# Optimization experiments

Measured on AMD Instinct MI355X. Metric: run time of the kernel, lower is better.

The kernel has to match this reference:

```python
import jax, jax.numpy as jnp
import numpy as np

NUM_HEADS = 16
NUM_KV_HEADS = 8
HEAD_DIM = 128
EPS = 1e-6
SLIDING_WINDOW = 1024
ROPE_THETA = 10000.0


def _rms_norm(x, w):
    # per-head RMSNorm in fp32, as in Qwen3RMSNorm
    xf = x.astype(jnp.float32)
    var = jnp.mean(xf * xf, axis=-1, keepdims=True)
    return (w * (xf * jax.lax.rsqrt(var + EPS))).astype(x.dtype)


def _rotate_half(x):
    d = x.shape[-1] // 2
    return jnp.concatenate([-x[..., d:], x[..., :d]], axis=-1)


def setup_inputs() -> dict:
    key = jax.random.key(0)
    ks = jax.random.split(key, 6)
    B, S, H = 2, 2048, 2048
    hidden_states = jax.random.normal(ks[0], (B, S, H), dtype=jnp.float32)
    # RoPE tables per HF convention: cos/sin of shape [B, S, head_dim]
    inv_freq = 1.0 / (ROPE_THETA ** (np.arange(0, HEAD_DIM, 2, dtype=np.float32) / HEAD_DIM))
    pos = np.arange(S, dtype=np.float32)
    ang = np.outer(pos, inv_freq)  # [S, HEAD_DIM/2]
    emb = np.concatenate([ang, ang], axis=-1)  # [S, HEAD_DIM]
    cos = jnp.broadcast_to(jnp.asarray(np.cos(emb)), (B, S, HEAD_DIM))
    sin = jnp.broadcast_to(jnp.asarray(np.sin(emb)), (B, S, HEAD_DIM))
    sc = 0.02
    Wq = jax.random.normal(ks[1], (NUM_HEADS * HEAD_DIM, H), dtype=jnp.float32) * sc
    Wk = jax.random.normal(ks[2], (NUM_KV_HEADS * HEAD_DIM, H), dtype=jnp.float32) * sc
    Wv = jax.random.normal(ks[3], (NUM_KV_HEADS * HEAD_DIM, H), dtype=jnp.float32) * sc
    Wo = jax.random.normal(ks[4], (H, NUM_HEADS * HEAD_DIM), dtype=jnp.float32) * sc
    q_norm_w = jnp.ones((HEAD_DIM,), dtype=jnp.float32)
    k_norm_w = jnp.ones((HEAD_DIM,), dtype=jnp.float32)
    return {"hidden_states": hidden_states, "cos": cos, "sin": sin,
            "Wq": Wq, "Wk": Wk, "Wv": Wv, "Wo": Wo,
            "q_norm_w": q_norm_w, "k_norm_w": k_norm_w}


def reference(hidden_states, cos, sin, Wq, Wk, Wv, Wo, q_norm_w, k_norm_w):
    B, S, H = hidden_states.shape
    scaling = HEAD_DIM ** -0.5
    # projections (torch Linear: y = x @ W.T), reshape to [B, nH, S, D]
    q = jnp.einsum('bsh,oh->bso', hidden_states, Wq).reshape(B, S, NUM_HEADS, HEAD_DIM)
    k = jnp.einsum('bsh,oh->bso', hidden_states, Wk).reshape(B, S, NUM_KV_HEADS, HEAD_DIM)
    v = jnp.einsum('bsh,oh->bso', hidden_states, Wv).reshape(B, S, NUM_KV_HEADS, HEAD_DIM)
    q = _rms_norm(q, q_norm_w).transpose(0, 2, 1, 3)  # [B, nH, S, D]
    k = _rms_norm(k, k_norm_w).transpose(0, 2, 1, 3)  # [B, nKV, S, D]
    v = v.transpose(0, 2, 1, 3)
    # RoPE, cos/sin broadcast over heads (unsqueeze_dim=1)
    c = cos[:, None, :, :]
    s = sin[:, None, :, :]
    q = q * c + _rotate_half(q) * s
    k = k * c + _rotate_half(k) * s
    # GQA: repeat kv heads
    groups = NUM_HEADS // NUM_KV_HEADS
    k = jnp.repeat(k, groups, axis=1)
    v = jnp.repeat(v, groups, axis=1)
    # causal + sliding-window mask
    i = jnp.arange(S)[:, None]
    j = jnp.arange(S)[None, :]
    mask = (j <= i) & (i - j < SLIDING_WINDOW)  # [S, S]
    scores = jnp.einsum('bhqd,bhkd->bhqk', q, k) * scaling
    scores = jnp.where(mask[None, None], scores, jnp.finfo(scores.dtype).min)
    probs = jax.nn.softmax(scores, axis=-1)
    attn = jnp.einsum('bhqk,bhkd->bhqd', probs, v)  # [B, nH, S, D]
    attn = attn.transpose(0, 2, 1, 3).reshape(B, S, NUM_HEADS * HEAD_DIM)
    out = jnp.einsum('bso,ho->bsh', attn, Wo)
    return out
```

## Files before the change

### kernel.cpp

```cpp
#include <hip/hip_runtime.h>
#include <stdint.h>

#define S_LEN 2048
#define BATCH 2
#define HID 2048
#define NH 16
#define NKV 8
#define HD 128
#define WINDOW 1024
#define SCALE 0.08838834764831845f
#define QKVW 4096

typedef unsigned short u16;
typedef unsigned int u32;
typedef __attribute__((ext_vector_type(8))) short short8;
typedef __attribute__((ext_vector_type(4))) float f32x4;
typedef __attribute__((ext_vector_type(16))) float f32x16;
typedef __attribute__((ext_vector_type(4))) u16 u16x4;

__device__ __forceinline__ u16 f2b(float f) {
  u32 u = __builtin_bit_cast(u32, f);
  return (u16)((u + 0x7fffu + ((u >> 16) & 1u)) >> 16);
}
__device__ __forceinline__ float b2f(u16 h) {
  u32 u = ((u32)h) << 16;
  return __builtin_bit_cast(float, u);
}
__device__ __forceinline__ u32 pk_bf16(float a, float b) {
  u32 d;
  asm("v_cvt_pk_bf16_f32 %0, %1, %2" : "=v"(d) : "v"(a), "v"(b));
  return d;
}

__device__ __forceinline__ void gload_lds16(const u16* g, u16* l) {
  __builtin_amdgcn_global_load_lds(
      (const __attribute__((address_space(1))) u32*)g,
      (__attribute__((address_space(3))) u32*)l, 16, 0, 0);
}

template <int N>
__device__ __forceinline__ void wait_vm() {
  if constexpr (N == 0) asm volatile("s_waitcnt vmcnt(0)" ::: "memory");
  else if constexpr (N == 2) asm volatile("s_waitcnt vmcnt(2)" ::: "memory");
  else if constexpr (N == 4) asm volatile("s_waitcnt vmcnt(4)" ::: "memory");
}

__global__ __launch_bounds__(256) void k_conv(const float* __restrict__ src,
                                              u16* __restrict__ dst, int n4) {
  int i = blockIdx.x * blockDim.x + threadIdx.x;
  int st = gridDim.x * blockDim.x;
  for (; i < n4; i += st) {
    f32x4 v = ((const f32x4*)src)[i];
    u16x4 o;
    o[0] = f2b(v[0]); o[1] = f2b(v[1]); o[2] = f2b(v[2]); o[3] = f2b(v[3]);
    ((u16x4*)dst)[i] = o;
  }
}

__device__ __forceinline__ void store_c(u16* C, long idx, float v) { C[idx] = f2b(v); }
__device__ __forceinline__ void store_c(float* C, long idx, float v) { C[idx] = v; }

#define LOADAF(MB)                                                          \
  _Pragma("unroll") for (int i_ = 0; i_ < 4; ++i_) {                        \
    af[i_][0] = *(const short8*)&sA[cur][arow + ((MB) + i_) * 1024 + akc0]; \
    af[i_][1] = *(const short8*)&sA[cur][arow + ((MB) + i_) * 1024 + akc1]; \
  }
#define LOADBF(NB)                                                          \
  _Pragma("unroll") for (int j_ = 0; j_ < 2; ++j_) {                        \
    bf[j_][0] = *(const short8*)&sB[cur][brow + ((NB) + j_) * 1024 + akc0]; \
    bf[j_][1] = *(const short8*)&sB[cur][brow + ((NB) + j_) * 1024 + akc1]; \
  }
#define STAGE_A(H)                                                    \
  gload_lds16(Abase + aOff[H][0] + koff, &sA[nxt][aDst[H][0]]);       \
  gload_lds16(Abase + aOff[H][1] + koff, &sA[nxt][aDst[H][1]]);
#define STAGE_B(H)                                                    \
  gload_lds16(Bbase + bOff[H][0] + koff, &sB[nxt][bDst[H][0]]);       \
  gload_lds16(Bbase + bOff[H][1] + koff, &sB[nxt][bDst[H][1]]);
#define MFMAQ(MI0, NI0)                                                         \
  __builtin_amdgcn_s_setprio(1);                                                \
  _Pragma("unroll") for (int i_ = 0; i_ < 4; ++i_) {                            \
    _Pragma("unroll") for (int j_ = 0; j_ < 2; ++j_) {                          \
      acc[(MI0) + i_][(NI0) + j_] = __builtin_amdgcn_mfma_f32_16x16x32_bf16(    \
          af[i_][0], bf[j_][0], acc[(MI0) + i_][(NI0) + j_], 0, 0, 0);          \
      acc[(MI0) + i_][(NI0) + j_] = __builtin_amdgcn_mfma_f32_16x16x32_bf16(    \
          af[i_][1], bf[j_][1], acc[(MI0) + i_][(NI0) + j_], 0, 0, 0);          \
    }                                                                           \
  }                                                                             \
  __builtin_amdgcn_s_setprio(0);
#define OPEN_MFMA()                                      \
  __builtin_amdgcn_sched_barrier(0);                     \
  __builtin_amdgcn_s_barrier();                          \
  asm volatile("s_waitcnt lgkmcnt(0)" ::: "memory");     \
  __builtin_amdgcn_sched_barrier(0);

template <typename OutT>
__global__ __launch_bounds__(512, 1) void k_gemm4p(const u16* __restrict__ A,
                                                   const u16* __restrict__ B,
                                                   OutT* __restrict__ C,
                                                   int M, int N, int K) {
  __shared__ u16 sA[2][256 * 64];
  __shared__ u16 sB[2][256 * 64];
  const int tid = threadIdx.x;
  const int lane = tid & 63;
  const int w = tid >> 6;
  const int l15 = lane & 15;
  const int lg = lane >> 4;
  const int wm = w >> 2;
  const int wn = w & 3;
  const int sw = l15 & 7;

  const int gx = gridDim.x;
  const int nwg = gx * gridDim.y;
  const int flat = blockIdx.y * gx + blockIdx.x;
  const int tile = (flat & 7) * (nwg >> 3) + (flat >> 3);
  const long m0 = (long)(tile / gx) * 256;
  const long n0 = (long)(tile % gx) * 256;

  const u16* Abase = A + m0 * K;
  const u16* Bbase = B + n0 * K;

  int aOff[2][2], aDst[2][2], bOff[2][2], bDst[2][2];
#pragma unroll
  for (int h = 0; h < 2; ++h)
#pragma unroll
    for (int i = 0; i < 2; ++i) {
      const int c = tid + i * 512;
      const int lr = c >> 3, chs = c & 7;
      const int grA = ((lr >> 6) << 7) + (h << 6) + (lr & 63);
      aOff[h][i] = grA * K + (chs ^ (grA & 7)) * 8;
      aDst[h][i] = grA * 64 + chs * 8;
      const int grB = ((lr >> 5) << 6) + (h << 5) + (lr & 31);
      bOff[h][i] = grB * K + (chs ^ (grB & 7)) * 8;
      bDst[h][i] = grB * 64 + chs * 8;
    }

  f32x4 acc[8][4];
  const f32x4 z4 = {0.f, 0.f, 0.f, 0.f};
#pragma unroll
  for (int i = 0; i < 8; ++i)
#pragma unroll
    for (int j = 0; j < 4; ++j) acc[i][j] = z4;

  const int arow = (wm * 128 + l15) * 64;
  const int brow = (wn * 64 + l15) * 64;
  const int akc0 = (lg ^ sw) * 8;
  const int akc1 = ((4 + lg) ^ sw) * 8;

  const int NT = K >> 6;
  int cur = 0;
  short8 af[4][2], bf[2][2];

  {
    const int nxt = 0, koff = 0;
    STAGE_A(0); STAGE_B(0); STAGE_B(1); STAGE_A(1);
  }
  wait_vm<4>();
  __builtin_amdgcn_s_barrier();

  for (int t = 0; t < NT - 1; ++t) {
    const int nxt = cur ^ 1;
    const int koff = (t + 1) * 64;
    LOADAF(0) LOADBF(0)
    STAGE_A(0)
    wait_vm<4>();
    OPEN_MFMA()
    MFMAQ(0, 0)
    __builtin_amdgcn_s_barrier();
    LOADBF(2)
    STAGE_B(0)
    wait_vm<4>();
    OPEN_MFMA()
    MFMAQ(0, 2)
    __builtin_amdgcn_s_barrier();
    LOADAF(4)
    STAGE_B(1)
    OPEN_MFMA()
    MFMAQ(4, 2)
    __builtin_amdgcn_s_barrier();
    LOADBF(0)
    STAGE_A(1)
    wait_vm<4>();
    OPEN_MFMA()
    MFMAQ(4, 0)
    __builtin_amdgcn_s_barrier();
    cur = nxt;
  }
  {
    LOADAF(0) LOADBF(0)
    wait_vm<2>();
    OPEN_MFMA()
    MFMAQ(0, 0)
    __builtin_amdgcn_s_barrier();
    LOADBF(2)
    wait_vm<0>();
    OPEN_MFMA()
    MFMAQ(0, 2)
    __builtin_amdgcn_s_barrier();
    LOADAF(4)
    OPEN_MFMA()
    MFMAQ(4, 2)
    __builtin_amdgcn_s_barrier();
    LOADBF(0)
    OPEN_MFMA()
    MFMAQ(4, 0)
    __builtin_amdgcn_s_barrier();
  }

#pragma unroll
  for (int mi = 0; mi < 8; ++mi)
#pragma unroll
    for (int ni = 0; ni < 4; ++ni)
#pragma unroll
      for (int r = 0; r < 4; ++r) {
        long row = m0 + wm * 128 + mi * 16 + lg * 4 + r;
        long col = n0 + wn * 64 + ni * 16 + l15;
        store_c(C, row * (long)N + col, acc[mi][ni][r]);
      }
}

__global__ __launch_bounds__(256) void k_normrope(u16* __restrict__ QKV,
                                                  const float* __restrict__ cosb,
                                                  const float* __restrict__ sinb,
                                                  const float* __restrict__ qw,
                                                  const float* __restrict__ kw) {
  const int lane = threadIdx.x & 63;
  const int w = threadIdx.x >> 6;
  int row = blockIdx.x * 4 + w;
  const int nQ = BATCH * S_LEN * NH;
  u16* p;
  const float* nw;
  int tok;
  float sc;
  if (row < nQ) {
    tok = row >> 4;
    int h = row & 15;
    p = QKV + (long)tok * QKVW + h * HD;
    nw = qw;
    sc = SCALE;
  } else {
    int r2 = row - nQ;
    tok = r2 >> 3;
    int h = r2 & 7;
    p = QKV + (long)tok * QKVW + 2048 + h * HD;
    nw = kw;
    sc = 1.0f;
  }
  float x0 = b2f(p[lane]);
  float x1 = b2f(p[lane + 64]);
  float ss = x0 * x0 + x1 * x1;
#pragma unroll
  for (int mk = 1; mk < 64; mk <<= 1) ss += __shfl_xor(ss, mk, 64);
  float rinv = rsqrtf(ss * (1.0f / 128.0f) + 1e-6f);
  float y0 = x0 * rinv * nw[lane];
  float y1 = x1 * rinv * nw[lane + 64];
  const float* cp = cosb + (long)tok * HD;
  const float* sp = sinb + (long)tok * HD;
  float o0 = (y0 * cp[lane] - y1 * sp[lane]) * sc;
  float o1 = (y1 * cp[lane + 64] + y0 * sp[lane + 64]) * sc;
  p[lane] = f2b(o0);
  p[lane + 64] = f2b(o1);
}

__global__ __launch_bounds__(256, 2) void k_attn(const u16* __restrict__ QKV,
                                                 u16* __restrict__ AO) {
  __shared__ u16 sK[64 * 128];
  __shared__ u16 sVT[64 * 128];
  const int tid = threadIdx.x;
  const int lane = tid & 63;
  const int l31 = lane & 31;
  const int hi = lane >> 5;
  const int w = tid >> 6;
  const int q0 = blockIdx.x * 128;
  const int h = blockIdx.y;
  const int b = blockIdx.z;
  const int kvh = h >> 1;
  const int qw0 = q0 + w * 32;
  const int iq = qw0 + l31;

  const long tokbase = (long)b * S_LEN;
  const u16* Qrow = QKV + (tokbase + qw0 + l31) * QKVW + h * HD;
  short8 qf[8];
#pragma unroll
  for (int dt = 0; dt < 8; ++dt) qf[dt] = *(const short8*)(Qrow + dt * 16 + hi * 8);

  f32x16 o[4];
#pragma unroll
  for (int n = 0; n < 4; ++n)
#pragma unroll
    for (int r = 0; r < 16; ++r) o[n][r] = 0.f;
  float m = 0.f, lsum = 0.f;

  const u16* Kbase = QKV + tokbase * QKVW + 2048 + kvh * HD;
  const u16* Vbase = QKV + tokbase * QKVW + 3072 + kvh * HD;

  int kc_row[4], kc_off[4];
  u16* kc_dst[4];
#pragma unroll
  for (int i = 0; i < 4; ++i) {
    const int c = tid + 256 * i;
    kc_row[i] = c >> 4;
    kc_off[i] = (((c & 15) ^ ((c >> 4) & 7))) * 8;
    kc_dst[i] = &sK[c * 8];
  }
  const int rp = tid & 31;
  const int dc0 = tid >> 5;
  const int rg_st = rp >> 2;

  int t_lo = q0 - (WINDOW - 1);
  t_lo = (t_lo < 0 ? 0 : t_lo) >> 6;
  const int t_hi = (q0 + 127) >> 6;

  for (int t = t_lo; t <= t_hi; ++t) {
    const int kv0 = t << 6;
#pragma unroll
    for (int i = 0; i < 4; ++i)
      gload_lds16(Kbase + (long)(kv0 + kc_row[i]) * QKVW + kc_off[i], kc_dst[i]);
#pragma unroll
    for (int i = 0; i < 2; ++i) {
      const int dc = dc0 + i * 8;
      const u16* vp = Vbase + (long)(kv0 + 2 * rp) * QKVW + dc * 8;
      short8 v0 = *(const short8*)vp;
      short8 v1 = *(const short8*)(vp + QKVW);
#pragma unroll
      for (int e = 0; e < 8; ++e) {
        const int d = dc * 8 + e;
        const int unit = d * 8 + (rg_st ^ (d & 7));
        ((u32*)sVT)[unit * 4 + (rp & 3)] = (u32)(u16)v0[e] | ((u32)(u16)v1[e] << 16);
      }
    }
    __syncthreads();

    const bool skipw = (kv0 > qw0 + 31) || (kv0 + 63 < qw0 - (WINDOW - 1));
    if (!skipw) {
      const bool full = (kv0 + 63 <= qw0) && ((qw0 + 31) - kv0 < WINDOW);
      f32x16 s0, s1;
#pragma unroll
      for (int r = 0; r < 16; ++r) { s0[r] = 0.f; s1[r] = 0.f; }
      const int rsw = l31 & 7;
#pragma unroll
      for (int dt = 0; dt < 8; ++dt) {
        const int ch = hi + 2 * dt;
        const short8 kf0 = *(const short8*)&sK[(l31 * 16 + (ch ^ rsw)) * 8];
        s0 = __builtin_amdgcn_mfma_f32_32x32x16_bf16(kf0, qf[dt], s0, 0, 0, 0);
        const short8 kf1 = *(const short8*)&sK[((l31 + 32) * 16 + (ch ^ rsw)) * 8];
        s1 = __builtin_amdgcn_mfma_f32_32x32x16_bf16(kf1, qf[dt], s1, 0, 0, 0);
      }
      float p[32];
#pragma unroll
      for (int r = 0; r < 16; ++r) { p[r] = s0[r]; p[16 + r] = s1[r]; }
      if (!full) {
#pragma unroll
        for (int r = 0; r < 32; ++r) {
          const int kk = kv0 + (r >> 4) * 32 + 4 * hi + (r & 3) + 8 * ((r >> 2) & 3);
          p[r] = ((u32)(iq - kk) < (u32)WINDOW) ? p[r] : -3.0e38f;
        }
      }
      float tm = p[0];
#pragma unroll
      for (int r = 1; r < 32; ++r) tm = fmaxf(tm, p[r]);
      tm = fmaxf(tm, __shfl_xor(tm, 32, 64));
      const float mn = fmaxf(m, tm);
      const float al = __expf(m - mn);
      m = mn;
      float rs = 0.f;
#pragma unroll
      for (int r = 0; r < 32; ++r) { p[r] = __expf(p[r] - mn); rs += p[r]; }
      rs += __shfl_xor(rs, 32, 64);
      lsum = lsum * al + rs;
#pragma unroll
      for (int n = 0; n < 4; ++n)
#pragma unroll
        for (int r = 0; r < 16; ++r) o[n][r] *= al;

      short8 pf[4];
#pragma unroll
      for (int ks = 0; ks < 4; ++ks) {
        const int bb = (ks >> 1) * 16 + (ks & 1) * 8;
        u32 a0 = pk_bf16(p[bb + 0], p[bb + 1]);
        u32 b0 = pk_bf16(p[bb + 4], p[bb + 5]);
        u32 a1 = pk_bf16(p[bb + 2], p[bb + 3]);
        u32 b1 = pk_bf16(p[bb + 6], p[bb + 7]);
        asm volatile("v_permlane32_swap_b32 %0, %1" : "+v"(a0), "+v"(b0));
        asm volatile("v_permlane32_swap_b32 %0, %1" : "+v"(a1), "+v"(b1));
        union { u32 u[4]; short8 s; } uu;
        uu.u[0] = a0; uu.u[1] = a1; uu.u[2] = b0; uu.u[3] = b1;
        pf[ks] = uu.s;
      }
#pragma unroll
      for (int dt = 0; dt < 4; ++dt) {
        const int d = l31 + 32 * dt;
        const int dsw = d & 7;
#pragma unroll
        for (int ks = 0; ks < 4; ++ks) {
          const int rg = ks * 2 + hi;
          const short8 vf = *(const short8*)&sVT[(d * 8 + (rg ^ dsw)) * 8];
          o[dt] = __builtin_amdgcn_mfma_f32_32x32x16_bf16(vf, pf[ks], o[dt], 0, 0, 0);
        }
      }
    }
    __syncthreads();
  }

  __syncthreads();
  float* R = ((float*)sK) + w * 1024;
  const float rl = 1.0f / lsum;
  const int half = hi;
#pragma unroll
  for (int dt = 0; dt < 4; ++dt) {
#pragma unroll
    for (int r = 0; r < 16; ++r) {
      const int dp = 4 * hi + (r & 3) + 8 * (r >> 2);
      R[dp * 32 + (l31 ^ (4 * (dp & 7)))] = o[dt][r] * rl;
    }
    __syncthreads();
    union { u16 hh[16]; short8 s[2]; } U;
#pragma unroll
    for (int j = 0; j < 16; ++j) {
      const int dp = half * 16 + j;
      U.hh[j] = f2b(R[dp * 32 + (l31 ^ (4 * (dp & 7)))]);
    }
    u16* dst = AO + (tokbase + q0 + w * 32 + l31) * (NH * HD) + h * HD + dt * 32 + half * 16;
    *(short8*)dst = U.s[0];
    *(short8*)(dst + 8) = U.s[1];
    __syncthreads();
  }
}

extern "C" void kernel_launch(void* const* d_in, const int* in_sizes, int n_in,
                              void* d_out, int out_size, void* d_ws, size_t ws_size,
                              hipStream_t stream) {
  const float* hs   = (const float*)d_in[0];
  const float* cosb = (const float*)d_in[1];
  const float* sinb = (const float*)d_in[2];
  const float* Wq   = (const float*)d_in[3];
  const float* Wk   = (const float*)d_in[4];
  const float* Wv   = (const float*)d_in[5];
  const float* Wo   = (const float*)d_in[6];
  const float* qw   = (const float*)d_in[7];
  const float* kw   = (const float*)d_in[8];
  float* out = (float*)d_out;

  const long SZ_X  = (long)BATCH * S_LEN * HID;
  const long SZ_WQ = (long)NH * HD * HID;
  const long SZ_WK = (long)NKV * HD * HID;
  u16* Xb   = (u16*)d_ws;
  u16* Wqb  = Xb + SZ_X;
  u16* Wkb  = Wqb + SZ_WQ;
  u16* Wvb  = Wkb + SZ_WK;
  u16* Wob  = Wvb + SZ_WK;
  u16* QKVb = Wob + SZ_WQ;
  u16* AOb  = QKVb + (long)BATCH * S_LEN * QKVW;

  k_conv<<<2048, 256, 0, stream>>>(hs, Xb, (int)(SZ_X / 4));
  k_conv<<<1024, 256, 0, stream>>>(Wq, Wqb, (int)(SZ_WQ / 4));
  k_conv<<<512, 256, 0, stream>>>(Wk, Wkb, (int)(SZ_WK / 4));
  k_conv<<<512, 256, 0, stream>>>(Wv, Wvb, (int)(SZ_WK / 4));
  k_conv<<<1024, 256, 0, stream>>>(Wo, Wob, (int)(SZ_WQ / 4));

  k_gemm4p<u16><<<dim3(16, 16), 512, 0, stream>>>(
      Xb, Wqb, QKVb, BATCH * S_LEN, QKVW, HID);

  k_normrope<<<(BATCH * S_LEN * (NH + NKV)) / 4, 256, 0, stream>>>(QKVb, cosb, sinb, qw, kw);

  k_attn<<<dim3(S_LEN / 128, NH, BATCH), 256, 0, stream>>>(QKVb, AOb);

  k_gemm4p<float><<<dim3(8, 16), 512, 0, stream>>>(
      AOb, Wob, out, BATCH * S_LEN, HID, HID);
}
```

Baseline: 232.4 us.

## Restructure GEMM into 8-phase pipeline and templatize N tile size

Replaces the 4-phase double-buffered GEMM loop with an 8-phase loop over two K-tiles per iteration. Stage loads are issued at half-buffer granularity, so the next tile's halves start loading as soon as the corresponding LDS region is free. The output-projection GEMM now uses a 256x128 tile, giving 256 workgroups instead of 128 for better CU occupancy on the device. This adds more barriers and harder-to-verify wait counts, and the smaller B tile lowers arithmetic intensity.

```diff
diff --git a/kernel.cpp b/kernel.cpp
--- a/kernel.cpp
+++ b/kernel.cpp
@@ -41,7 +41,7 @@
 template <int N>
 __device__ __forceinline__ void wait_vm() {
   if constexpr (N == 0) asm volatile("s_waitcnt vmcnt(0)" ::: "memory");
-  else if constexpr (N == 2) asm volatile("s_waitcnt vmcnt(2)" ::: "memory");
+  else if constexpr (N == 3) asm volatile("s_waitcnt vmcnt(3)" ::: "memory");
   else if constexpr (N == 4) asm volatile("s_waitcnt vmcnt(4)" ::: "memory");
 }
 
@@ -60,30 +60,30 @@
 __device__ __forceinline__ void store_c(u16* C, long idx, float v) { C[idx] = f2b(v); }
 __device__ __forceinline__ void store_c(float* C, long idx, float v) { C[idx] = v; }
 
-#define LOADAF(MB)                                                          \
-  _Pragma("unroll") for (int i_ = 0; i_ < 4; ++i_) {                        \
-    af[i_][0] = *(const short8*)&sA[cur][arow + ((MB) + i_) * 1024 + akc0]; \
-    af[i_][1] = *(const short8*)&sA[cur][arow + ((MB) + i_) * 1024 + akc1]; \
-  }
-#define LOADBF(NB)                                                          \
-  _Pragma("unroll") for (int j_ = 0; j_ < 2; ++j_) {                        \
-    bf[j_][0] = *(const short8*)&sB[cur][brow + ((NB) + j_) * 1024 + akc0]; \
-    bf[j_][1] = *(const short8*)&sB[cur][brow + ((NB) + j_) * 1024 + akc1]; \
-  }
-#define STAGE_A(H)                                                    \
-  gload_lds16(Abase + aOff[H][0] + koff, &sA[nxt][aDst[H][0]]);       \
-  gload_lds16(Abase + aOff[H][1] + koff, &sA[nxt][aDst[H][1]]);
-#define STAGE_B(H)                                                    \
-  gload_lds16(Bbase + bOff[H][0] + koff, &sB[nxt][bDst[H][0]]);       \
-  gload_lds16(Bbase + bOff[H][1] + koff, &sB[nxt][bDst[H][1]]);
-#define MFMAQ(MI0, NI0)                                                         \
+#define LOADAF(BUF, MQ)                                                         \
+  _Pragma("unroll") for (int i_ = 0; i_ < 4; ++i_) {                            \
+    af[i_][0] = *(const short8*)&sA[BUF][arow + ((MQ)*64 + i_*16) * 64 + akc0]; \
+    af[i_][1] = *(const short8*)&sA[BUF][arow + ((MQ)*64 + i_*16) * 64 + akc1]; \
+  }
+#define LOADBF(BUF, NQ)                                                         \
+  _Pragma("unroll") for (int j_ = 0; j_ < NIH; ++j_) {                          \
+    bf[j_][0] = *(const short8*)&sB[BUF][brow + ((NQ)*QB + j_*16) * 64 + akc0]; \
+    bf[j_][1] = *(const short8*)&sB[BUF][brow + ((NQ)*QB + j_*16) * 64 + akc1]; \
+  }
+#define STAGE_A(H, BUF, KT)                                            \
+  _Pragma("unroll") for (int i_ = 0; i_ < 2; ++i_)                     \
+      gload_lds16(Abase + aOff[H][i_] + (KT) * 64, &sA[BUF][aDst[H][i_]]);
+#define STAGE_B(H, BUF, KT)                                            \
+  _Pragma("unroll") for (int i_ = 0; i_ < BL; ++i_)                    \
+      gload_lds16(Bbase + bOff[H][i_] + (KT) * 64, &sB[BUF][bDst[H][i_]]);
+#define MFMAQ(MQ, NQ)                                                           \
   __builtin_amdgcn_s_setprio(1);                                                \
   _Pragma("unroll") for (int i_ = 0; i_ < 4; ++i_) {                            \
-    _Pragma("unroll") for (int j_ = 0; j_ < 2; ++j_) {                          \
-      acc[(MI0) + i_][(NI0) + j_] = __builtin_amdgcn_mfma_f32_16x16x32_bf16(    \
-          af[i_][0], bf[j_][0], acc[(MI0) + i_][(NI0) + j_], 0, 0, 0);          \
-      acc[(MI0) + i_][(NI0) + j_] = __builtin_amdgcn_mfma_f32_16x16x32_bf16(    \
-          af[i_][1], bf[j_][1], acc[(MI0) + i_][(NI0) + j_], 0, 0, 0);          \
+    _Pragma("unroll") for (int j_ = 0; j_ < NIH; ++j_) {                        \
+      acc[(MQ)*4 + i_][(NQ)*NIH + j_] = __builtin_amdgcn_mfma_f32_16x16x32_bf16(\
+          af[i_][0], bf[j_][0], acc[(MQ)*4 + i_][(NQ)*NIH + j_], 0, 0, 0);      \
+      acc[(MQ)*4 + i_][(NQ)*NIH + j_] = __builtin_amdgcn_mfma_f32_16x16x32_bf16(\
+          af[i_][1], bf[j_][1], acc[(MQ)*4 + i_][(NQ)*NIH + j_], 0, 0, 0);      \
     }                                                                           \
   }                                                                             \
   __builtin_amdgcn_s_setprio(0);
@@ -92,14 +92,23 @@
   __builtin_amdgcn_s_barrier();                          \
   asm volatile("s_waitcnt lgkmcnt(0)" ::: "memory");     \
   __builtin_amdgcn_sched_barrier(0);
-
-template <typename OutT>
-__global__ __launch_bounds__(512, 1) void k_gemm4p(const u16* __restrict__ A,
+#define CLOSEP()                                         \
+  __builtin_amdgcn_s_barrier();                          \
+  __builtin_amdgcn_sched_barrier(0);
+
+template <int BN, typename OutT>
+__global__ __launch_bounds__(512, 1) void k_gemm8p(const u16* __restrict__ A,
                                                    const u16* __restrict__ B,
                                                    OutT* __restrict__ C,
                                                    int M, int N, int K) {
+  constexpr int NIH = BN / 128;
+  constexpr int NI = 2 * NIH;
+  constexpr int BL = BN / 128;
+  constexpr int QB = BN / 8;
+  constexpr int WV = 2 + BL;
+
   __shared__ u16 sA[2][256 * 64];
-  __shared__ u16 sB[2][256 * 64];
+  __shared__ u16 sB[2][BN * 64];
   const int tid = threadIdx.x;
   const int lane = tid & 63;
   const int w = tid >> 6;
@@ -114,14 +123,14 @@
   const int flat = blockIdx.y * gx + blockIdx.x;
   const int tile = (flat & 7) * (nwg >> 3) + (flat >> 3);
   const long m0 = (long)(tile / gx) * 256;
-  const long n0 = (long)(tile % gx) * 256;
+  const long n0 = (long)(tile % gx) * BN;
 
   const u16* Abase = A + m0 * K;
   const u16* Bbase = B + n0 * K;
 
   int aOff[2][2], aDst[2][2], bOff[2][2], bDst[2][2];
 #pragma unroll
-  for (int h = 0; h < 2; ++h)
+  for (int h = 0; h < 2; ++h) {
 #pragma unroll
     for (int i = 0; i < 2; ++i) {
       const int c = tid + i * 512;
@@ -129,91 +138,130 @@
       const int grA = ((lr >> 6) << 7) + (h << 6) + (lr & 63);
       aOff[h][i] = grA * K + (chs ^ (grA & 7)) * 8;
       aDst[h][i] = grA * 64 + chs * 8;
-      const int grB = ((lr >> 5) << 6) + (h << 5) + (lr & 31);
+    }
+#pragma unroll
+    for (int i = 0; i < BL; ++i) {
+      const int c = tid + i * 512;
+      const int lr = c >> 3, chs = c & 7;
+      const int grB = (lr / QB) * (2 * QB) + h * QB + (lr % QB);
       bOff[h][i] = grB * K + (chs ^ (grB & 7)) * 8;
       bDst[h][i] = grB * 64 + chs * 8;
     }
-
-  f32x4 acc[8][4];
+  }
+
+  f32x4 acc[8][NI];
   const f32x4 z4 = {0.f, 0.f, 0.f, 0.f};
 #pragma unroll
   for (int i = 0; i < 8; ++i)
 #pragma unroll
-    for (int j = 0; j < 4; ++j) acc[i][j] = z4;
+    for (int j = 0; j < NI; ++j) acc[i][j] = z4;
 
   const int arow = (wm * 128 + l15) * 64;
-  const int brow = (wn * 64 + l15) * 64;
+  const int brow = (wn * (BN / 4) + l15) * 64;
   const int akc0 = (lg ^ sw) * 8;
   const int akc1 = ((4 + lg) ^ sw) * 8;
 
   const int NT = K >> 6;
-  int cur = 0;
-  short8 af[4][2], bf[2][2];
-
+  const int NIT = NT >> 1;
+  short8 af[4][2], bf[NIH][2];
+
+  STAGE_A(0, 0, 0) STAGE_B(0, 0, 0) STAGE_B(1, 0, 0) STAGE_A(1, 0, 0)
+  STAGE_A(0, 1, 1) STAGE_B(1, 1, 1)
+  wait_vm<WV>();
+  CLOSEP()
+
+  for (int it = 0; it < NIT - 1; ++it) {
+    const int u = 2 * it;
+    LOADAF(0, 0) LOADBF(0, 0)
+    STAGE_A(1, 1, u + 1)
+    OPEN_MFMA()
+    MFMAQ(0, 0)
+    CLOSEP()
+    LOADBF(0, 1)
+    STAGE_B(0, 1, u + 1)
+    OPEN_MFMA()
+    MFMAQ(0, 1)
+    CLOSEP()
+    LOADAF(0, 1)
+    STAGE_A(0, 0, u + 2)
+    OPEN_MFMA()
+    MFMAQ(1, 1)
+    CLOSEP()
+    LOADBF(0, 0)
+    STAGE_B(1, 0, u + 2)
+    wait_vm<WV>();
+    OPEN_MFMA()
+    MFMAQ(1, 0)
+    CLOSEP()
+    LOADAF(1, 0) LOADBF(1, 0)
+    STAGE_A(1, 0, u + 2)
+    OPEN_MFMA()
+    MFMAQ(0, 0)
+    CLOSEP()
+    LOADBF(1, 1)
+    STAGE_B(0, 0, u + 2)
+    OPEN_MFMA()
+    MFMAQ(0, 1)
+    CLOSEP()
+    LOADAF(1, 1)
+    STAGE_A(0, 1, u + 3)
+    OPEN_MFMA()
+    MFMAQ(1, 1)
+    CLOSEP()
+    LOADBF(1, 0)
+    STAGE_B(1, 1, u + 3)
+    wait_vm<WV>();
+    OPEN_MFMA()
+    MFMAQ(1, 0)
+    CLOSEP()
+  }
   {
-    const int nxt = 0, koff = 0;
-    STAGE_A(0); STAGE_B(0); STAGE_B(1); STAGE_A(1);
-  }
-  wait_vm<4>();
-  __builtin_amdgcn_s_barrier();
-
-  for (int t = 0; t < NT - 1; ++t) {
-    const int nxt = cur ^ 1;
-    const int koff = (t + 1) * 64;
-    LOADAF(0) LOADBF(0)
-    STAGE_A(0)
-    wait_vm<4>();
+    const int u = NT - 2;
+    LOADAF(0, 0) LOADBF(0, 0)
+    STAGE_A(1, 1, u + 1)
     OPEN_MFMA()
     MFMAQ(0, 0)
-    __builtin_amdgcn_s_barrier();
-    LOADBF(2)
-    STAGE_B(0)
-    wait_vm<4>();
-    OPEN_MFMA()
-    MFMAQ(0, 2)
-    __builtin_amdgcn_s_barrier();
-    LOADAF(4)
-    STAGE_B(1)
-    OPEN_MFMA()
-    MFMAQ(4, 2)
-    __builtin_amdgcn_s_barrier();
-    LOADBF(0)
-    STAGE_A(1)
-    wait_vm<4>();
-    OPEN_MFMA()
-    MFMAQ(4, 0)
-    __builtin_amdgcn_s_barrier();
-    cur = nxt;
-  }
-  {
-    LOADAF(0) LOADBF(0)
-    wait_vm<2>();
+    CLOSEP()
+    LOADBF(0, 1)
+    STAGE_B(0, 1, u + 1)
+    OPEN_MFMA()
+    MFMAQ(0, 1)
+    CLOSEP()
+    LOADAF(0, 1)
+    OPEN_MFMA()
+    MFMAQ(1, 1)
+    CLOSEP()
+    LOADBF(0, 0)
+    wait_vm<0>();
+    OPEN_MFMA()
+    MFMAQ(1, 0)
+    CLOSEP()
+    LOADAF(1, 0) LOADBF(1, 0)
     OPEN_MFMA()
     MFMAQ(0, 0)
-    __builtin_amdgcn_s_barrier();
-    LOADBF(2)
-    wait_vm<0>();
-    OPEN_MFMA()
-    MFMAQ(0, 2)
-    __builtin_amdgcn_s_barrier();
-    LOADAF(4)
-    OPEN_MFMA()
-    MFMAQ(4, 2)
-    __builtin_amdgcn_s_barrier();
-    LOADBF(0)
-    OPEN_MFMA()
-    MFMAQ(4, 0)
-    __builtin_amdgcn_s_barrier();
+    CLOSEP()
+    LOADBF(1, 1)
+    OPEN_MFMA()
+    MFMAQ(0, 1)
+    CLOSEP()
+    LOADAF(1, 1)
+    OPEN_MFMA()
+    MFMAQ(1, 1)
+    CLOSEP()
+    LOADBF(1, 0)
+    OPEN_MFMA()
+    MFMAQ(1, 0)
+    CLOSEP()
   }
 
 #pragma unroll
   for (int mi = 0; mi < 8; ++mi)
 #pragma unroll
-    for (int ni = 0; ni < 4; ++ni)
+    for (int ni = 0; ni < NI; ++ni)
 #pragma unroll
       for (int r = 0; r < 4; ++r) {
         long row = m0 + wm * 128 + mi * 16 + lg * 4 + r;
-        long col = n0 + wn * 64 + ni * 16 + l15;
+        long col = n0 + wn * (BN / 4) + ni * 16 + l15;
         store_c(C, row * (long)N + col, acc[mi][ni][r]);
       }
 }
@@ -457,13 +505,13 @@
   k_conv<<<512, 256, 0, stream>>>(Wv, Wvb, (int)(SZ_WK / 4));
   k_conv<<<1024, 256, 0, stream>>>(Wo, Wob, (int)(SZ_WQ / 4));
 
-  k_gemm4p<u16><<<dim3(16, 16), 512, 0, stream>>>(
+  k_gemm8p<256, u16><<<dim3(16, 16), 512, 0, stream>>>(
       Xb, Wqb, QKVb, BATCH * S_LEN, QKVW, HID);
 
   k_normrope<<<(BATCH * S_LEN * (NH + NKV)) / 4, 256, 0, stream>>>(QKVb, cosb, sinb, qw, kw);
 
   k_attn<<<dim3(S_LEN / 128, NH, BATCH), 256, 0, stream>>>(QKVb, AOb);
 
-  k_gemm4p<float><<<dim3(8, 16), 512, 0, stream>>>(
+  k_gemm8p<128, float><<<dim3(16, 16), 512, 0, stream>>>(
       AOb, Wob, out, BATCH * S_LEN, HID, HID);
 }
```

After: 213.4 us. 8.2% less time.
